# Optimization experiments

Measured on AMD Instinct MI355X. Metric: run time of the kernel, lower is better.

## Reference

```python
import jax, jax.numpy as jnp
import numpy as np

NEG = float(-2**32 + 1)  # mask fill value used by the original module
H = 8  # number of heads (matches init kwarg h)


def setup_inputs() -> dict:
    key = jax.random.key(0)
    B, S, D, Q, V = 4, 2048, 512, 64, 64
    ks = jax.random.split(key, 10)
    sc = 1.0 / np.sqrt(D)
    x = jax.random.normal(ks[0], (B, S, D), jnp.float32)
    padding_mask = jax.random.randint(ks[1], (B, S), 0, 2, jnp.int32)
    Wq = jax.random.normal(ks[2], (H * Q, D), jnp.float32) * sc
    bq = jnp.zeros((H * Q,), jnp.float32)
    Wk = jax.random.normal(ks[3], (H * Q, D), jnp.float32) * sc
    bk = jnp.zeros((H * Q,), jnp.float32)
    Wv = jax.random.normal(ks[4], (H * V, D), jnp.float32) * sc
    bv = jnp.zeros((H * V,), jnp.float32)
    Wo = jax.random.normal(ks[5], (D, H * V), jnp.float32) * (1.0 / np.sqrt(H * V))
    bo = jnp.zeros((D,), jnp.float32)
    return {"x": x, "padding_mask": padding_mask, "Wq": Wq, "bq": bq,
            "Wk": Wk, "bk": bk, "Wv": Wv, "bv": bv, "Wo": Wo, "bo": bo}


def reference(x, padding_mask, Wq, bq, Wk, bk, Wv, bv, Wo, bo):
    # stage is hardcoded to 'train' (mask=True in init), so the causal branch runs.
    B, S, D = x.shape
    q_dim = Wq.shape[0] // H
    v_dim = Wv.shape[0] // H

    def split_heads(t, d):
        # torch: cat(chunk(h, dim=-1), dim=0) -> head-major [H*B, S, d]
        return t.reshape(B, S, H, d).transpose(2, 0, 1, 3).reshape(H * B, S, d)

    Qh = split_heads(x @ Wq.T + bq, q_dim)   # [H*B, S, q]
    Kh = split_heads(x @ Wk.T + bk, q_dim)
    Vh = split_heads(x @ Wv.T + bv, v_dim)

    score = jnp.einsum('nsd,ntd->nst', Qh, Kh) / jnp.sqrt(jnp.float32(q_dim))  # [H*B,S,S]
    pre_score = score  # module returns the UNMASKED scores (saved before masking)

    # causal mask (mask=True, stage=='train')
    causal = jnp.tril(jnp.ones((S, S), jnp.float32))
    score = jnp.where(causal > 0, score, NEG)

    # padding mask: built batch-major [B*H,S,S] while score is head-major [H*B,...]
    # -- faithful reproduction of the original ordering quirk.
    pm = jnp.broadcast_to(padding_mask[:, None, None, :], (B, H, S, S)).reshape(B * H, S, S)
    score = jnp.where(pm == 0, NEG, score)

    attn = jax.nn.softmax(score, axis=-1)
    out = jnp.einsum('nst,ntd->nsd', attn, Vh)  # [H*B, S, v]

    # torch: cat(chunk(h, dim=0), dim=-1) -> [B, S, H*v]
    heads = out.reshape(H, B, S, v_dim).transpose(1, 2, 0, 3).reshape(B, S, H * v_dim)
    self_attention = heads @ Wo.T + bo
    return self_attention, pre_score
```

## Files before the change

### kernel.cpp

```cpp
#include <hip/hip_runtime.h>
#include <hip/hip_fp16.h>
#include <math.h>

typedef _Float16 f16;
typedef _Float16 f16x8 __attribute__((ext_vector_type(8)));
typedef _Float16 f16x4 __attribute__((ext_vector_type(4)));
typedef float    f32x4 __attribute__((ext_vector_type(4)));

#define MFMA16(a,b,c) __builtin_amdgcn_mfma_f32_16x16x32_f16(a, b, c, 0, 0, 0)

#define MASKNEG (-6.0e9f)
#define LOG2E   1.44269504088896f

__global__ __launch_bounds__(256) void qkv_gemm(
    const float* __restrict__ x,
    const float* __restrict__ Wq, const float* __restrict__ bq,
    const float* __restrict__ Wk, const float* __restrict__ bk,
    const float* __restrict__ Wv, const float* __restrict__ bv,
    f16* __restrict__ Qws, f16* __restrict__ Kws, f16* __restrict__ Vt)
{
    __shared__ f16 Al[128 * 48];
    __shared__ f16 Wl[64 * 48];

    const int tid = threadIdx.x;
    const int bx  = blockIdx.x;
    const int m0  = blockIdx.y * 128;
    const int widx = bx >> 3;
    const int n0   = (bx & 7) * 64;

    const float* W    = (widx == 0) ? Wq : (widx == 1) ? Wk : Wv;
    const float* bias = (widx == 0) ? bq : (widx == 1) ? bk : bv;

    const int wid = tid >> 6, lane = tid & 63;
    const int g = lane >> 4, c = lane & 15;
    const int wm = (wid >> 1) * 64, wn = (wid & 1) * 32;

    const int sr = tid >> 3, sc = tid & 7;

    f32x4 acc[4][2] = {};

    for (int kk = 0; kk < 512; kk += 32) {
        __syncthreads();
        #pragma unroll
        for (int rr = 0; rr < 4; ++rr) {
            int row = sr + rr * 32;
            float4 v = *(const float4*)&x[(size_t)(m0 + row) * 512 + kk + sc * 4];
            f16x4 h4 = {(f16)v.x, (f16)v.y, (f16)v.z, (f16)v.w};
            *(f16x4*)&Al[row * 48 + sc * 4] = h4;
        }
        #pragma unroll
        for (int rr = 0; rr < 2; ++rr) {
            int row = sr + rr * 32;
            float4 v = *(const float4*)&W[(size_t)(n0 + row) * 512 + kk + sc * 4];
            f16x4 h4 = {(f16)v.x, (f16)v.y, (f16)v.z, (f16)v.w};
            *(f16x4*)&Wl[row * 48 + sc * 4] = h4;
        }
        __syncthreads();

        f16x8 b0 = *(const f16x8*)&Wl[(wn +  0 + c) * 48 + g * 8];
        f16x8 b1 = *(const f16x8*)&Wl[(wn + 16 + c) * 48 + g * 8];
        #pragma unroll
        for (int mf = 0; mf < 4; ++mf) {
            f16x8 a = *(const f16x8*)&Al[(wm + mf * 16 + c) * 48 + g * 8];
            acc[mf][0] = MFMA16(a, b0, acc[mf][0]);
            acc[mf][1] = MFMA16(a, b1, acc[mf][1]);
        }
    }

    #pragma unroll
    for (int nf = 0; nf < 2; ++nf) {
        int cc = n0 + wn + nf * 16 + c;
        float bval = bias[cc];
        #pragma unroll
        for (int mf = 0; mf < 4; ++mf) {
            if (widx < 2) {
                f16* outp = (widx == 0) ? Qws : Kws;
                #pragma unroll
                for (int r = 0; r < 4; ++r) {
                    int mrow = m0 + wm + mf * 16 + g * 4 + r;
                    outp[(size_t)mrow * 512 + cc] = (f16)(acc[mf][nf][r] + bval);
                }
            } else {
                int h  = n0 >> 6;
                int d  = wn + nf * 16 + c;
                int t0 = m0 + wm + mf * 16 + g * 4;
                int b  = t0 >> 11;
                int ts = t0 & 2047;
                int nn = h * 4 + b;
                f16x4 pk = {(f16)(acc[mf][nf][0] + bval), (f16)(acc[mf][nf][1] + bval),
                            (f16)(acc[mf][nf][2] + bval), (f16)(acc[mf][nf][3] + bval)};
                *(f16x4*)&Vt[((size_t)(nn * 64 + d)) * 2048 + ts] = pk;
            }
        }
    }
}

__global__ __launch_bounds__(256) void vsum_kernel(
    const f16* __restrict__ Vt, float* __restrict__ Vsum)
{
    const int row  = blockIdx.x * 4 + (threadIdx.x >> 6);
    const int lane = threadIdx.x & 63;
    const f16* p = Vt + (size_t)row * 2048;
    float s = 0.f;
    #pragma unroll
    for (int i = 0; i < 4; ++i) {
        f16x8 v = *(const f16x8*)&p[i * 512 + lane * 8];
        #pragma unroll
        for (int j = 0; j < 8; ++j) s += (float)v[j];
    }
    #pragma unroll
    for (int off = 1; off < 64; off <<= 1) s += __shfl_xor(s, off, 64);
    if (lane == 0) Vsum[row] = s;
}

__global__ __launch_bounds__(256) void attn_kernel(
    const f16* __restrict__ Qws, const f16* __restrict__ Kws,
    const f16* __restrict__ Vt,  const int* __restrict__ pmask,
    const float* __restrict__ Vsum,
    float* __restrict__ pre_score, f16* __restrict__ attn_out)
{
    __shared__ f16 Kl[64 * 72];
    __shared__ f16 Vl[64 * 72];
    __shared__ f16 Pl[4][32 * 72];

    const int tid = threadIdx.x;
    const int wid = tid >> 6, lane = tid & 63;
    const int g = lane >> 4, c = lane & 15;
    const int qt = blockIdx.x;
    const int n  = blockIdx.y;
    const int h = n >> 2, b = n & 3;
    const int pmrow = n >> 3;
    const int q0 = qt * 128 + wid * 32;
    const int live = 2 * qt + 2;

    f16x8 qf[2][2];
    #pragma unroll
    for (int mi = 0; mi < 2; ++mi)
        #pragma unroll
        for (int ks = 0; ks < 2; ++ks)
            qf[mi][ks] = *(const f16x8*)
                &Qws[(size_t)(b * 2048 + q0 + mi * 16 + c) * 512 + h * 64 + ks * 32 + g * 8];

    f32x4 o[2][4] = {};
    float mrow[2][4], lrow[2][4];
    #pragma unroll
    for (int mi = 0; mi < 2; ++mi)
        #pragma unroll
        for (int r = 0; r < 4; ++r) { mrow[mi][r] = -INFINITY; lrow[mi][r] = 0.0f; }

    const int sr = tid >> 3, sc = tid & 7;
    const int* pmp = pmask + pmrow * 2048;
    const f16* Kbase = Kws + (size_t)(b * 2048) * 512 + h * 64;
    const f16* Vbase = Vt + (size_t)(n * 64) * 2048;

    for (int kt = 0; kt < live; ++kt) {
        __syncthreads();
        #pragma unroll
        for (int rr = 0; rr < 2; ++rr) {
            int row = sr + rr * 32;
            *(uint4*)&Kl[row * 72 + sc * 8] =
                *(const uint4*)&Kbase[(size_t)(kt * 64 + row) * 512 + sc * 8];
            *(uint4*)&Vl[row * 72 + sc * 8] =
                *(const uint4*)&Vbase[(size_t)row * 2048 + kt * 64 + sc * 8];
        }
        __syncthreads();

        f32x4 s[2][4] = {};
        #pragma unroll
        for (int nf = 0; nf < 4; ++nf)
            #pragma unroll
            for (int ks = 0; ks < 2; ++ks) {
                f16x8 kf = *(const f16x8*)&Kl[(nf * 16 + c) * 72 + ks * 32 + g * 8];
                s[0][nf] = MFMA16(qf[0][ks], kf, s[0][nf]);
                s[1][nf] = MFMA16(qf[1][ks], kf, s[1][nf]);
            }

        #pragma unroll
        for (int nf = 0; nf < 4; ++nf) {
            int tg  = kt * 64 + nf * 16 + c;
            int pmv = pmp[tg];
            #pragma unroll
            for (int mi = 0; mi < 2; ++mi)
                #pragma unroll
                for (int r = 0; r < 4; ++r) {
                    float v = s[mi][nf][r] * 0.125f;
                    int srow = q0 + mi * 16 + g * 4 + r;
                    __builtin_nontemporal_store(
                        v, &pre_score[((size_t)n * 2048 + srow) * 2048 + tg]);
                    s[mi][nf][r] = (tg <= srow && pmv != 0) ? v * LOG2E : MASKNEG;
                }
        }

        float alpha[2][4];
        #pragma unroll
        for (int mi = 0; mi < 2; ++mi)
            #pragma unroll
            for (int r = 0; r < 4; ++r) {
                float rm = fmaxf(fmaxf(s[mi][0][r], s[mi][1][r]),
                                 fmaxf(s[mi][2][r], s[mi][3][r]));
                rm = fmaxf(rm, __shfl_xor(rm, 1, 64));
                rm = fmaxf(rm, __shfl_xor(rm, 2, 64));
                rm = fmaxf(rm, __shfl_xor(rm, 4, 64));
                rm = fmaxf(rm, __shfl_xor(rm, 8, 64));
                float mn = fmaxf(mrow[mi][r], rm);
                alpha[mi][r] = exp2f(mrow[mi][r] - mn);
                mrow[mi][r] = mn;
            }
        #pragma unroll
        for (int mi = 0; mi < 2; ++mi) {
            float rs[4] = {0.f, 0.f, 0.f, 0.f};
            #pragma unroll
            for (int nf = 0; nf < 4; ++nf)
                #pragma unroll
                for (int r = 0; r < 4; ++r) {
                    float p = exp2f(s[mi][nf][r] - mrow[mi][r]);
                    rs[r] += p;
                    Pl[wid][(mi * 16 + g * 4 + r) * 72 + nf * 16 + c] = (f16)p;
                }
            #pragma unroll
            for (int r = 0; r < 4; ++r) {
                float t = rs[r];
                t += __shfl_xor(t, 1, 64);
                t += __shfl_xor(t, 2, 64);
                t += __shfl_xor(t, 4, 64);
                t += __shfl_xor(t, 8, 64);
                lrow[mi][r] = lrow[mi][r] * alpha[mi][r] + t;
                #pragma unroll
                for (int dn = 0; dn < 4; ++dn) o[mi][dn][r] *= alpha[mi][r];
            }
        }
        asm volatile("s_waitcnt lgkmcnt(0)" ::: "memory");

        #pragma unroll
        for (int ks = 0; ks < 2; ++ks) {
            f16x8 pa0 = *(const f16x8*)&Pl[wid][( 0 + c) * 72 + ks * 32 + g * 8];
            f16x8 pa1 = *(const f16x8*)&Pl[wid][(16 + c) * 72 + ks * 32 + g * 8];
            #pragma unroll
            for (int dn = 0; dn < 4; ++dn) {
                f16x8 vb = *(const f16x8*)&Vl[(dn * 16 + c) * 72 + ks * 32 + g * 8];
                o[0][dn] = MFMA16(pa0, vb, o[0][dn]);
                o[1][dn] = MFMA16(pa1, vb, o[1][dn]);
            }
        }
    }

    for (int kt = live; kt < 32; ++kt) {
        __syncthreads();
        #pragma unroll
        for (int rr = 0; rr < 2; ++rr) {
            int row = sr + rr * 32;
            *(uint4*)&Kl[row * 72 + sc * 8] =
                *(const uint4*)&Kbase[(size_t)(kt * 64 + row) * 512 + sc * 8];
        }
        __syncthreads();

        f32x4 s[2][4] = {};
        #pragma unroll
        for (int nf = 0; nf < 4; ++nf)
            #pragma unroll
            for (int ks = 0; ks < 2; ++ks) {
                f16x8 kf = *(const f16x8*)&Kl[(nf * 16 + c) * 72 + ks * 32 + g * 8];
                s[0][nf] = MFMA16(qf[0][ks], kf, s[0][nf]);
                s[1][nf] = MFMA16(qf[1][ks], kf, s[1][nf]);
            }
        #pragma unroll
        for (int nf = 0; nf < 4; ++nf) {
            int tg = kt * 64 + nf * 16 + c;
            #pragma unroll
            for (int mi = 0; mi < 2; ++mi)
                #pragma unroll
                for (int r = 0; r < 4; ++r) {
                    int srow = q0 + mi * 16 + g * 4 + r;
                    __builtin_nontemporal_store(s[mi][nf][r] * 0.125f,
                        &pre_score[((size_t)n * 2048 + srow) * 2048 + tg]);
                }
        }
    }

    #pragma unroll
    for (int mi = 0; mi < 2; ++mi)
        #pragma unroll
        for (int r = 0; r < 4; ++r) {
            int srow = q0 + mi * 16 + g * 4 + r;
            bool dead = (mrow[mi][r] == MASKNEG);
            float inv_l = dead ? 0.f : 1.0f / lrow[mi][r];
            #pragma unroll
            for (int dn = 0; dn < 4; ++dn) {
                float val = dead ? Vsum[n * 64 + dn * 16 + c] * (1.0f / 2048.0f)
                                 : o[mi][dn][r] * inv_l;
                attn_out[(size_t)(b * 2048 + srow) * 512 + h * 64 + dn * 16 + c] = (f16)val;
            }
        }
}

__global__ __launch_bounds__(256) void out_gemm(
    const f16* __restrict__ Aattn, const float* __restrict__ Wo,
    const float* __restrict__ bo, float* __restrict__ outp)
{
    __shared__ f16 Al[128 * 48];
    __shared__ f16 Wl[64 * 48];

    const int tid = threadIdx.x;
    const int n0 = blockIdx.x * 64;
    const int m0 = blockIdx.y * 128;
    const int wid = tid >> 6, lane = tid & 63;
    const int g = lane >> 4, c = lane & 15;
    const int wm = (wid >> 1) * 64, wn = (wid & 1) * 32;

    const int sr4 = tid >> 2, sc4 = tid & 3;
    const int sr8 = tid >> 3, sc8 = tid & 7;

    f32x4 acc[4][2] = {};

    for (int kk = 0; kk < 512; kk += 32) {
        __syncthreads();
        #pragma unroll
        for (int rr = 0; rr < 2; ++rr) {
            int row = sr4 + rr * 64;
            *(uint4*)&Al[row * 48 + sc4 * 8] =
                *(const uint4*)&Aattn[(size_t)(m0 + row) * 512 + kk + sc4 * 8];
        }
        #pragma unroll
        for (int rr = 0; rr < 2; ++rr) {
            int row = sr8 + rr * 32;
            float4 v = *(const float4*)&Wo[(size_t)(n0 + row) * 512 + kk + sc8 * 4];
            f16x4 h4 = {(f16)v.x, (f16)v.y, (f16)v.z, (f16)v.w};
            *(f16x4*)&Wl[row * 48 + sc8 * 4] = h4;
        }
        __syncthreads();

        f16x8 b0 = *(const f16x8*)&Wl[(wn +  0 + c) * 48 + g * 8];
        f16x8 b1 = *(const f16x8*)&Wl[(wn + 16 + c) * 48 + g * 8];
        #pragma unroll
        for (int mf = 0; mf < 4; ++mf) {
            f16x8 a = *(const f16x8*)&Al[(wm + mf * 16 + c) * 48 + g * 8];
            acc[mf][0] = MFMA16(a, b0, acc[mf][0]);
            acc[mf][1] = MFMA16(a, b1, acc[mf][1]);
        }
    }

    #pragma unroll
    for (int nf = 0; nf < 2; ++nf) {
        int cc = n0 + wn + nf * 16 + c;
        float bval = bo[cc];
        #pragma unroll
        for (int mf = 0; mf < 4; ++mf)
            #pragma unroll
            for (int r = 0; r < 4; ++r)
                outp[(size_t)(m0 + wm + mf * 16 + g * 4 + r) * 512 + cc] =
                    acc[mf][nf][r] + bval;
    }
}

extern "C" void kernel_launch(void* const* d_in, const int* in_sizes, int n_in,
                              void* d_out, int out_size, void* d_ws, size_t ws_size,
                              hipStream_t stream)
{
    (void)in_sizes; (void)n_in; (void)out_size; (void)ws_size;

    const float* x  = (const float*)d_in[0];
    const int*   pm = (const int*)  d_in[1];
    const float* Wq = (const float*)d_in[2];
    const float* bq = (const float*)d_in[3];
    const float* Wk = (const float*)d_in[4];
    const float* bk = (const float*)d_in[5];
    const float* Wv = (const float*)d_in[6];
    const float* bv = (const float*)d_in[7];
    const float* Wo = (const float*)d_in[8];
    const float* bo = (const float*)d_in[9];

    float* out = (float*)d_out;
    float* pre = out + (size_t)4 * 2048 * 512;

    f16*   Qws  = (f16*)d_ws;
    f16*   Kws  = Qws + (size_t)8192 * 512;
    f16*   Vt   = Kws + (size_t)8192 * 512;
    f16*   Aat  = Vt  + (size_t)2048 * 2048;
    float* Vsum = (float*)(Aat + (size_t)8192 * 512);

    qkv_gemm   <<<dim3(24, 64), 256, 0, stream>>>(x, Wq, bq, Wk, bk, Wv, bv, Qws, Kws, Vt);
    vsum_kernel<<<dim3(512),    256, 0, stream>>>(Vt, Vsum);
    attn_kernel<<<dim3(16, 32), 256, 0, stream>>>(Qws, Kws, Vt, pm, Vsum, pre, Aat);
    out_gemm   <<<dim3(8, 64),  256, 0, stream>>>(Aat, Wo, bo, out);
}
```

Baseline: 337.0 us.

## Pair low and high causal query tiles per block to balance attention work

Each attention block now owns a 64-row query tile from the start of the sequence and the mirrored 64-row tile from the end, instead of 128 contiguous rows. Every block therefore does about the same amount of causal softmax and PV work, which removes the tail where late-sequence blocks ran up to 32 live tiles while early ones ran 2. The softmax/PV body becomes a lambda with per-half liveness flags. The fully masked trailing tiles now read K directly from global memory and skip the LDS staging and barriers. The risk is more uncoalesced global K reads in that tail loop and some register pressure from the lambda.

```diff
diff --git a/kernel.cpp b/kernel.cpp
--- a/kernel.cpp
+++ b/kernel.cpp
@@ -130,16 +130,17 @@
     const int n  = blockIdx.y;
     const int h = n >> 2, b = n & 3;
     const int pmrow = n >> 3;
-    const int q0 = qt * 128 + wid * 32;
-    const int live = 2 * qt + 2;
+    const int qlo = qt * 64 + wid * 16;
+    const int qhi = (31 - qt) * 64 + wid * 16;
 
     f16x8 qf[2][2];
     #pragma unroll
-    for (int mi = 0; mi < 2; ++mi)
-        #pragma unroll
-        for (int ks = 0; ks < 2; ++ks)
-            qf[mi][ks] = *(const f16x8*)
-                &Qws[(size_t)(b * 2048 + q0 + mi * 16 + c) * 512 + h * 64 + ks * 32 + g * 8];
+    for (int ks = 0; ks < 2; ++ks) {
+        qf[0][ks] = *(const f16x8*)
+            &Qws[(size_t)(b * 2048 + qlo + c) * 512 + h * 64 + ks * 32 + g * 8];
+        qf[1][ks] = *(const f16x8*)
+            &Qws[(size_t)(b * 2048 + qhi + c) * 512 + h * 64 + ks * 32 + g * 8];
+    }
 
     f32x4 o[2][4] = {};
     float mrow[2][4], lrow[2][4];
@@ -152,8 +153,10 @@
     const int* pmp = pmask + pmrow * 2048;
     const f16* Kbase = Kws + (size_t)(b * 2048) * 512 + h * 64;
     const f16* Vbase = Vt + (size_t)(n * 64) * 2048;
-
-    for (int kt = 0; kt < live; ++kt) {
+    float* prow0 = pre_score + ((size_t)n * 2048 + qlo + g * 4) * 2048;
+    float* prow1 = pre_score + ((size_t)n * 2048 + qhi + g * 4) * 2048;
+
+    auto tile = [&](int kt, bool L0, bool L1) __attribute__((always_inline)) {
         __syncthreads();
         #pragma unroll
         for (int rr = 0; rr < 2; ++rr) {
@@ -180,20 +183,23 @@
             int tg  = kt * 64 + nf * 16 + c;
             int pmv = pmp[tg];
             #pragma unroll
-            for (int mi = 0; mi < 2; ++mi)
-                #pragma unroll
-                for (int r = 0; r < 4; ++r) {
-                    float v = s[mi][nf][r] * 0.125f;
-                    int srow = q0 + mi * 16 + g * 4 + r;
-                    __builtin_nontemporal_store(
-                        v, &pre_score[((size_t)n * 2048 + srow) * 2048 + tg]);
-                    s[mi][nf][r] = (tg <= srow && pmv != 0) ? v * LOG2E : MASKNEG;
-                }
-        }
-
-        float alpha[2][4];
-        #pragma unroll
-        for (int mi = 0; mi < 2; ++mi)
+            for (int r = 0; r < 4; ++r) {
+                float v0 = s[0][nf][r] * 0.125f;
+                float v1 = s[1][nf][r] * 0.125f;
+                __builtin_nontemporal_store(v0, &prow0[(size_t)r * 2048 + tg]);
+                __builtin_nontemporal_store(v1, &prow1[(size_t)r * 2048 + tg]);
+                if (L0) s[0][nf][r] = (tg <= qlo + g * 4 + r && pmv != 0)
+                                    ? v0 * LOG2E : MASKNEG;
+                if (L1) s[1][nf][r] = (tg <= qhi + g * 4 + r && pmv != 0)
+                                    ? v1 * LOG2E : MASKNEG;
+            }
+        }
+
+        #pragma unroll
+        for (int mi = 0; mi < 2; ++mi) {
+            if (mi == 0 && !L0) continue;
+            if (mi == 1 && !L1) continue;
+            float alpha[4];
             #pragma unroll
             for (int r = 0; r < 4; ++r) {
                 float rm = fmaxf(fmaxf(s[mi][0][r], s[mi][1][r]),
@@ -203,11 +209,9 @@
                 rm = fmaxf(rm, __shfl_xor(rm, 4, 64));
                 rm = fmaxf(rm, __shfl_xor(rm, 8, 64));
                 float mn = fmaxf(mrow[mi][r], rm);
-                alpha[mi][r] = exp2f(mrow[mi][r] - mn);
+                alpha[r] = exp2f(mrow[mi][r] - mn);
                 mrow[mi][r] = mn;
             }
-        #pragma unroll
-        for (int mi = 0; mi < 2; ++mi) {
             float rs[4] = {0.f, 0.f, 0.f, 0.f};
             #pragma unroll
             for (int nf = 0; nf < 4; ++nf)
@@ -224,42 +228,38 @@
                 t += __shfl_xor(t, 2, 64);
                 t += __shfl_xor(t, 4, 64);
                 t += __shfl_xor(t, 8, 64);
-                lrow[mi][r] = lrow[mi][r] * alpha[mi][r] + t;
+                lrow[mi][r] = lrow[mi][r] * alpha[r] + t;
                 #pragma unroll
-                for (int dn = 0; dn < 4; ++dn) o[mi][dn][r] *= alpha[mi][r];
+                for (int dn = 0; dn < 4; ++dn) o[mi][dn][r] *= alpha[r];
             }
         }
         asm volatile("s_waitcnt lgkmcnt(0)" ::: "memory");
 
         #pragma unroll
         for (int ks = 0; ks < 2; ++ks) {
-            f16x8 pa0 = *(const f16x8*)&Pl[wid][( 0 + c) * 72 + ks * 32 + g * 8];
-            f16x8 pa1 = *(const f16x8*)&Pl[wid][(16 + c) * 72 + ks * 32 + g * 8];
+            f16x8 pa0, pa1;
+            if (L0) pa0 = *(const f16x8*)&Pl[wid][( 0 + c) * 72 + ks * 32 + g * 8];
+            if (L1) pa1 = *(const f16x8*)&Pl[wid][(16 + c) * 72 + ks * 32 + g * 8];
             #pragma unroll
             for (int dn = 0; dn < 4; ++dn) {
                 f16x8 vb = *(const f16x8*)&Vl[(dn * 16 + c) * 72 + ks * 32 + g * 8];
-                o[0][dn] = MFMA16(pa0, vb, o[0][dn]);
-                o[1][dn] = MFMA16(pa1, vb, o[1][dn]);
-            }
-        }
-    }
-
-    for (int kt = live; kt < 32; ++kt) {
-        __syncthreads();
-        #pragma unroll
-        for (int rr = 0; rr < 2; ++rr) {
-            int row = sr + rr * 32;
-            *(uint4*)&Kl[row * 72 + sc * 8] =
-                *(const uint4*)&Kbase[(size_t)(kt * 64 + row) * 512 + sc * 8];
-        }
-        __syncthreads();
-
+                if (L0) o[0][dn] = MFMA16(pa0, vb, o[0][dn]);
+                if (L1) o[1][dn] = MFMA16(pa1, vb, o[1][dn]);
+            }
+        }
+    };
+
+    for (int kt = 0; kt <= qt; ++kt)          tile(kt, true,  true);
+    for (int kt = qt + 1; kt <= 31 - qt; ++kt) tile(kt, false, true);
+
+    for (int kt = 32 - qt; kt < 32; ++kt) {
         f32x4 s[2][4] = {};
         #pragma unroll
         for (int nf = 0; nf < 4; ++nf)
             #pragma unroll
             for (int ks = 0; ks < 2; ++ks) {
-                f16x8 kf = *(const f16x8*)&Kl[(nf * 16 + c) * 72 + ks * 32 + g * 8];
+                f16x8 kf = *(const f16x8*)
+                    &Kbase[(size_t)(kt * 64 + nf * 16 + c) * 512 + ks * 32 + g * 8];
                 s[0][nf] = MFMA16(qf[0][ks], kf, s[0][nf]);
                 s[1][nf] = MFMA16(qf[1][ks], kf, s[1][nf]);
             }
@@ -267,21 +267,21 @@
         for (int nf = 0; nf < 4; ++nf) {
             int tg = kt * 64 + nf * 16 + c;
             #pragma unroll
-            for (int mi = 0; mi < 2; ++mi)
-                #pragma unroll
-                for (int r = 0; r < 4; ++r) {
-                    int srow = q0 + mi * 16 + g * 4 + r;
-                    __builtin_nontemporal_store(s[mi][nf][r] * 0.125f,
-                        &pre_score[((size_t)n * 2048 + srow) * 2048 + tg]);
-                }
-        }
-    }
-
-    #pragma unroll
-    for (int mi = 0; mi < 2; ++mi)
+            for (int r = 0; r < 4; ++r) {
+                __builtin_nontemporal_store(s[0][nf][r] * 0.125f,
+                                            &prow0[(size_t)r * 2048 + tg]);
+                __builtin_nontemporal_store(s[1][nf][r] * 0.125f,
+                                            &prow1[(size_t)r * 2048 + tg]);
+            }
+        }
+    }
+
+    #pragma unroll
+    for (int mi = 0; mi < 2; ++mi) {
+        int qb = mi ? qhi : qlo;
         #pragma unroll
         for (int r = 0; r < 4; ++r) {
-            int srow = q0 + mi * 16 + g * 4 + r;
+            int srow = qb + g * 4 + r;
             bool dead = (mrow[mi][r] == MASKNEG);
             float inv_l = dead ? 0.f : 1.0f / lrow[mi][r];
             #pragma unroll
@@ -291,6 +291,7 @@
                 attn_out[(size_t)(b * 2048 + srow) * 512 + h * 64 + dn * 16 + c] = (f16)val;
             }
         }
+    }
 }
 
 __global__ __launch_bounds__(256) void out_gemm(
```

After: 308.4 us. 8.5% less time.
